# Optimization experiments

Hardware: AMD Instinct MI355X
Metric: run time of the kernel (lower is better)

The kernel has to match this reference:

```python
import jax, jax.numpy as jnp
import numpy as np

A_CONST = 0.4
C_CONST = 500.0
N_BINS = 10


def entropy(w):
    # Faithful to the torch helper: n=10 half-open bins [min+i*s, min+(i+1)*s);
    # the maximum element falls outside the last bin, as in the original.
    x = w.reshape(-1)
    lo = x.min()
    hi = x.max()
    scale = (hi - lo) / N_BINS
    i = jnp.arange(N_BINS, dtype=x.dtype)
    lower = lo + i * scale            # [n]
    upper = lo + (i + 1.0) * scale    # [n]
    in_bin = (x[None, :] >= lower[:, None]) & (x[None, :] < upper[:, None])  # [n, len]
    p = jnp.sum(in_bin, axis=1).astype(jnp.float32) / x.shape[0]
    return jnp.sum(jnp.where(p > 0, -p * jnp.log(p), 0.0))


def blend_weight(base_w, graft_w, pnet_w):
    # param_direction = |base - graft| passed through bias-free Linear(in, in)
    d = jnp.abs(base_w - graft_w) @ pnet_w.T          # [out, in]
    w_local = jax.nn.sigmoid(d)
    w_global = A_CONST / jnp.pi * jnp.arctan(C_CONST * (entropy(base_w) - entropy(graft_w))) + 0.5
    w_base = w_global * (1.0 - jnp.exp(-w_global * w_local))
    w_graft = (1.0 - w_global) * (1.0 - jnp.exp(-(1.0 - w_global) * (1.0 - w_local)))
    ws = jax.nn.softmax(jnp.stack([w_base, w_graft], axis=-1), axis=-1)  # [out, in, 2]
    return base_w * ws[..., 0] + graft_w * ws[..., 1]


def setup_inputs() -> dict:
    key = jax.random.key(0)
    ks = jax.random.split(key, 9)
    B, D_IN, D_H, D_OUT = 65536, 1024, 512, 1
    return {
        "x": jax.random.normal(ks[0], (B, D_IN), dtype=jnp.float32),
        "w0": jax.random.normal(ks[1], (D_H, D_IN), dtype=jnp.float32) * 0.05,
        "b0": jax.random.normal(ks[2], (D_H,), dtype=jnp.float32) * 0.05,
        "w1": jax.random.normal(ks[3], (D_OUT, D_H), dtype=jnp.float32) * 0.05,
        "b1": jax.random.normal(ks[4], (D_OUT,), dtype=jnp.float32) * 0.05,
        "p0": jax.random.normal(ks[5], (D_IN, D_IN), dtype=jnp.float32) * 0.05,
        "p1": jax.random.normal(ks[6], (D_H, D_H), dtype=jnp.float32) * 0.05,
        "g0": jax.random.normal(ks[7], (D_H, D_IN), dtype=jnp.float32) * 0.05,
        "g1": jax.random.normal(ks[8], (D_OUT, D_H), dtype=jnp.float32) * 0.05,
    }


def reference(x, w0, b0, w1, b1, p0, p1, g0, g1):
    W0 = blend_weight(w0, g0, p0)
    x = jax.nn.relu(x @ W0.T + b0)   # layer 0 + ReLU
    W1 = blend_weight(w1, g1, p1)
    x = x @ W1.T + b1                # layer 1, no activation
    return x
```

## Files before the change

kernel.cpp:

```cpp
#include <hip/hip_runtime.h>
#include <hip/hip_bf16.h>
#include <math.h>


typedef __attribute__((ext_vector_type(8))) short short8;
typedef __attribute__((ext_vector_type(4))) short short4v;
typedef __attribute__((ext_vector_type(4))) float floatx4;
typedef unsigned short ushort_t;

#define WS_ENT 0
#define WS_MM 4
#define WS_CNT 16
#define WS_W0B_WORD 64
#define WS_W1B_WORD (64 + 262144)

__device__ __forceinline__ unsigned f2ord(float f) {
    unsigned u = __float_as_uint(f);
    return (u & 0x80000000u) ? ~u : (u | 0x80000000u);
}
__device__ __forceinline__ float ord2f(unsigned k) {
    unsigned u = (k & 0x80000000u) ? (k ^ 0x80000000u) : ~k;
    return __uint_as_float(u);
}
__device__ __forceinline__ short f2bf(float f) {
    union { __hip_bfloat16 h; short s; } u;
    u.h = __float2bfloat16(f);
    return u.s;
}
__device__ __forceinline__ float blend_factor(float d, float wg) {
    float wl = 1.0f / (1.0f + expf(-d));
    float wb = wg * (1.0f - expf(-wg * wl));
    float wgr = (1.0f - wg) * (1.0f - expf(-(1.0f - wg) * (1.0f - wl)));
    return 1.0f / (1.0f + expf(-(wb - wgr)));
}
__device__ __forceinline__ float wglobal_from_ent(float eb, float eg) {
    return 0.12732395447351627f * atanf(500.0f * (eb - eg)) + 0.5f;
}
__device__ __forceinline__ void async16(const void* g, void* s) {
    __builtin_amdgcn_global_load_lds(
        (const __attribute__((address_space(1))) unsigned int*)g,
        (__attribute__((address_space(3))) unsigned int*)s, 16, 0, 0);
}

__global__ void init_ws(unsigned* ws_u) {
    int t = threadIdx.x;
    if (t < 4) {
        ws_u[WS_MM + 2 * t] = 0xFFFFFFFFu;
        ws_u[WS_MM + 2 * t + 1] = 0u;
    }
    if (t >= WS_CNT && t < WS_CNT + 40) ws_u[t] = 0u;
}

__device__ __forceinline__ void array_map(int bx, const float* w0, const float* g0,
                                          const float* w1, const float* g1,
                                          int& a, const float*& arr, int& per, int& start) {
    if (bx < 64) { a = 0; arr = w0; per = 524288 / 64; start = bx * per; }
    else if (bx < 128) { a = 1; arr = g0; per = 524288 / 64; start = (bx - 64) * per; }
    else if (bx == 128) { a = 2; arr = w1; per = 512; start = 0; }
    else { a = 3; arr = g1; per = 512; start = 0; }
}

__global__ __launch_bounds__(256) void minmax_kernel(const float* __restrict__ w0,
                                                     const float* __restrict__ g0,
                                                     const float* __restrict__ w1,
                                                     const float* __restrict__ g1,
                                                     unsigned* ws_u) {
    int a, per, start;
    const float* arr;
    array_map(blockIdx.x, w0, g0, w1, g1, a, arr, per, start);
    float mn = INFINITY, mx = -INFINITY;
    for (int i = threadIdx.x; i < per; i += 256) {
        float v = arr[start + i];
        mn = fminf(mn, v);
        mx = fmaxf(mx, v);
    }
#pragma unroll
    for (int off = 32; off > 0; off >>= 1) {
        mn = fminf(mn, __shfl_xor(mn, off));
        mx = fmaxf(mx, __shfl_xor(mx, off));
    }
    __shared__ float smn[4], smx[4];
    int wave = threadIdx.x >> 6, lane = threadIdx.x & 63;
    if (lane == 0) { smn[wave] = mn; smx[wave] = mx; }
    __syncthreads();
    if (threadIdx.x == 0) {
        mn = fminf(fminf(smn[0], smn[1]), fminf(smn[2], smn[3]));
        mx = fmaxf(fmaxf(smx[0], smx[1]), fmaxf(smx[2], smx[3]));
        atomicMin(&ws_u[WS_MM + 2 * a], f2ord(mn));
        atomicMax(&ws_u[WS_MM + 2 * a + 1], f2ord(mx));
    }
}

__global__ __launch_bounds__(256) void hist_kernel(const float* __restrict__ w0,
                                                   const float* __restrict__ g0,
                                                   const float* __restrict__ w1,
                                                   const float* __restrict__ g1,
                                                   unsigned* ws_u) {
    int a, per, start;
    const float* arr;
    array_map(blockIdx.x, w0, g0, w1, g1, a, arr, per, start);
    float lo = ord2f(ws_u[WS_MM + 2 * a]);
    float hi = ord2f(ws_u[WS_MM + 2 * a + 1]);
    float scale = __fdiv_rn(__fsub_rn(hi, lo), 10.0f);
    float lw[11];
#pragma unroll
    for (int j = 0; j < 11; j++)
        lw[j] = __fadd_rn(lo, __fmul_rn((float)j, scale));
    unsigned c[10];
#pragma unroll
    for (int b = 0; b < 10; b++) c[b] = 0u;
    for (int i = threadIdx.x; i < per; i += 256) {
        float v = arr[start + i];
#pragma unroll
        for (int b = 0; b < 10; b++)
            c[b] += (v >= lw[b] && v < lw[b + 1]) ? 1u : 0u;
    }
#pragma unroll
    for (int b = 0; b < 10; b++) {
#pragma unroll
        for (int off = 32; off > 0; off >>= 1) c[b] += __shfl_xor(c[b], off);
    }
    int lane = threadIdx.x & 63;
    if (lane == 0) {
#pragma unroll
        for (int b = 0; b < 10; b++)
            if (c[b] > 0u) atomicAdd(&ws_u[WS_CNT + a * 10 + b], c[b]);
    }
}

__global__ void finalize_ent_kernel(unsigned* ws_u) {
    int a = threadIdx.x;
    if (a < 4) {
        float n = (a < 2) ? 524288.0f : 512.0f;
        float ent = 0.0f;
        for (int i = 0; i < 10; i++) {
            float p = __fdiv_rn((float)ws_u[WS_CNT + a * 10 + i], n);
            if (p > 0.0f) ent = __fsub_rn(ent, __fmul_rn(p, logf(p)));
        }
        ((float*)ws_u)[WS_ENT + a] = ent;
    }
}

__global__ __launch_bounds__(256) void blend0_kernel(const float* __restrict__ w0,
                                                     const float* __restrict__ g0,
                                                     const float* __restrict__ p0,
                                                     const float* __restrict__ ws_f,
                                                     ushort_t* __restrict__ W0bb) {
    __shared__ ushort_t As[32 * 40];
    __shared__ ushort_t Ps[64 * 40];
    int tid = threadIdx.x;
    int w = tid >> 6, l = tid & 63;
    int bo = blockIdx.y * 32;
    int bi = blockIdx.x * 64;
    int wo = w & 1, wi = w >> 1;
    int m_in = l & 15, kq = l >> 4;

    floatx4 acc[2];
    const floatx4 zero = {0.0f, 0.0f, 0.0f, 0.0f};
    acc[0] = zero; acc[1] = zero;

    int ar = tid >> 3, ac = (tid & 7) * 4;
    int pr = tid >> 2, pc = (tid & 3) * 8;
    const float* wbase = w0 + (size_t)(bo + ar) * 1024 + ac;
    const float* gbase = g0 + (size_t)(bo + ar) * 1024 + ac;
    const float* pbase = p0 + (size_t)(bi + pr) * 1024 + pc;
    ushort_t* awr = &As[ar * 40 + ac];
    ushort_t* pwr = &Ps[pr * 40 + pc];

#pragma unroll 1
    for (int k0 = 0; k0 < 1024; k0 += 32) {
        float4 vw = *(const float4*)(wbase + k0);
        float4 vg = *(const float4*)(gbase + k0);
        float4 q0 = *(const float4*)(pbase + k0);
        float4 q1 = *(const float4*)(pbase + k0 + 4);
        short4v a4;
        a4[0] = f2bf(fabsf(vw.x - vg.x));
        a4[1] = f2bf(fabsf(vw.y - vg.y));
        a4[2] = f2bf(fabsf(vw.z - vg.z));
        a4[3] = f2bf(fabsf(vw.w - vg.w));
        short8 p8;
        p8[0] = f2bf(q0.x); p8[1] = f2bf(q0.y); p8[2] = f2bf(q0.z); p8[3] = f2bf(q0.w);
        p8[4] = f2bf(q1.x); p8[5] = f2bf(q1.y); p8[6] = f2bf(q1.z); p8[7] = f2bf(q1.w);
        *(short4v*)awr = a4;
        *(short8*)pwr = p8;
        __syncthreads();
        short8 af = *(const short8*)&As[(wo * 16 + m_in) * 40 + kq * 8];
        short8 pf0 = *(const short8*)&Ps[(wi * 32 + m_in) * 40 + kq * 8];
        short8 pf1 = *(const short8*)&Ps[(wi * 32 + 16 + m_in) * 40 + kq * 8];
        acc[0] = __builtin_amdgcn_mfma_f32_16x16x32_bf16(af, pf0, acc[0], 0, 0, 0);
        acc[1] = __builtin_amdgcn_mfma_f32_16x16x32_bf16(af, pf1, acc[1], 0, 0, 0);
        __syncthreads();
    }
    float wg = wglobal_from_ent(ws_f[WS_ENT + 0], ws_f[WS_ENT + 1]);
#pragma unroll
    for (int tn = 0; tn < 2; tn++) {
#pragma unroll
        for (int reg = 0; reg < 4; reg++) {
            int o = bo + wo * 16 + kq * 4 + reg;
            int i = bi + wi * 32 + tn * 16 + m_in;
            float s0 = blend_factor(acc[tn][reg], wg);
            float v = w0[o * 1024 + i] * s0 + g0[o * 1024 + i] * (1.0f - s0);
            W0bb[o * 1024 + i] = (ushort_t)f2bf(v);
        }
    }
}

__global__ __launch_bounds__(256) void blend1_kernel(const float* __restrict__ w1,
                                                     const float* __restrict__ g1,
                                                     const float* __restrict__ p1,
                                                     const float* __restrict__ ws_f,
                                                     float* __restrict__ W1b) {
    __shared__ float diff[512];
    int tid = threadIdx.x;
    for (int i = tid; i < 512; i += 256) diff[i] = fabsf(w1[i] - g1[i]);
    __syncthreads();
    int wave = tid >> 6, lane = tid & 63;
    int i = blockIdx.x * 4 + wave;
    float acc = 0.0f;
#pragma unroll
    for (int j = 0; j < 8; j++) {
        int k = lane + 64 * j;
        acc += diff[k] * p1[i * 512 + k];
    }
#pragma unroll
    for (int off = 32; off > 0; off >>= 1) acc += __shfl_xor(acc, off);
    if (lane == 0) {
        float wg = wglobal_from_ent(ws_f[WS_ENT + 2], ws_f[WS_ENT + 3]);
        float s0 = blend_factor(acc, wg);
        W1b[i] = w1[i] * s0 + g1[i] * (1.0f - s0);
    }
}

__global__ __launch_bounds__(256, 2) void main_mfma(const float* __restrict__ x,
                                                    const float* __restrict__ b0,
                                                    const ushort_t* __restrict__ W0bb,
                                                    const float* __restrict__ W1b,
                                                    const float* __restrict__ b1,
                                                    float* __restrict__ out) {
    __shared__ ushort_t As[64 * 40];
    __shared__ ushort_t Bs[512 * 32];
    __shared__ float red[4][64];
    int tid = threadIdx.x;
    int w = tid >> 6, l = tid & 63;
    int row0 = blockIdx.x * 64;
    int m_in = l & 15, kq = l >> 4;

    floatx4 acc[4][8];
    const floatx4 zero = {0.0f, 0.0f, 0.0f, 0.0f};
#pragma unroll
    for (int tm = 0; tm < 4; tm++)
#pragma unroll
        for (int tn = 0; tn < 8; tn++) acc[tm][tn] = zero;

    int arow = tid >> 2, acol = (tid & 3) * 8;
    const float* xbase = x + (size_t)(row0 + arow) * 1024 + acol;
    ushort_t* awr = &As[arow * 40 + acol];
    const ushort_t* bsrc = W0bb + (size_t)(w * 16 + (l >> 2)) * 1024 + (l & 3) * 8;
    ushort_t* bdst = &Bs[w * 512];

    float4 pv0 = *(const float4*)(xbase);
    float4 pv1 = *(const float4*)(xbase + 4);

#pragma unroll 1
    for (int k0 = 0; k0 < 1024; k0 += 32) {
#pragma unroll
        for (int r = 0; r < 8; r++)
            async16(bsrc + r * 65536 + k0, bdst + r * 2048);
        short8 s0;
        s0[0] = f2bf(pv0.x); s0[1] = f2bf(pv0.y); s0[2] = f2bf(pv0.z); s0[3] = f2bf(pv0.w);
        s0[4] = f2bf(pv1.x); s0[5] = f2bf(pv1.y); s0[6] = f2bf(pv1.z); s0[7] = f2bf(pv1.w);
        *(short8*)awr = s0;
        int kn = (k0 + 32 < 1024) ? k0 + 32 : 0;
        __syncthreads();
        pv0 = *(const float4*)(xbase + kn);
        pv1 = *(const float4*)(xbase + kn + 4);
        short8 af[4];
#pragma unroll
        for (int tm = 0; tm < 4; tm++)
            af[tm] = *(const short8*)&As[(tm * 16 + m_in) * 40 + kq * 8];
#pragma unroll
        for (int tn = 0; tn < 8; tn++) {
            short8 bfr = *(const short8*)&Bs[(w * 128 + tn * 16 + m_in) * 32 + kq * 8];
#pragma unroll
            for (int tm = 0; tm < 4; tm++)
                acc[tm][tn] = __builtin_amdgcn_mfma_f32_16x16x32_bf16(
                    af[tm], bfr, acc[tm][tn], 0, 0, 0);
        }
        __syncthreads();
    }

    float b0v[8], w1v[8];
#pragma unroll
    for (int tn = 0; tn < 8; tn++) {
        int h = w * 128 + tn * 16 + m_in;
        b0v[tn] = b0[h];
        w1v[tn] = W1b[h];
    }
#pragma unroll
    for (int tm = 0; tm < 4; tm++) {
#pragma unroll
        for (int reg = 0; reg < 4; reg++) {
            float s = 0.0f;
#pragma unroll
            for (int tn = 0; tn < 8; tn++) {
                float y = acc[tm][tn][reg] + b0v[tn];
                y = fmaxf(y, 0.0f);
                s += y * w1v[tn];
            }
            s += __shfl_xor(s, 1);
            s += __shfl_xor(s, 2);
            s += __shfl_xor(s, 4);
            s += __shfl_xor(s, 8);
            if (m_in == 0) red[w][tm * 16 + kq * 4 + reg] = s;
        }
    }
    __syncthreads();
    if (tid < 64)
        out[row0 + tid] = red[0][tid] + red[1][tid] + red[2][tid] + red[3][tid] + b1[0];
}

extern "C" void kernel_launch(void* const* d_in, const int* in_sizes, int n_in,
                              void* d_out, int out_size, void* d_ws, size_t ws_size,
                              hipStream_t stream) {
    const float* x = (const float*)d_in[0];
    const float* w0 = (const float*)d_in[1];
    const float* b0 = (const float*)d_in[2];
    const float* w1 = (const float*)d_in[3];
    const float* b1 = (const float*)d_in[4];
    const float* p0 = (const float*)d_in[5];
    const float* p1 = (const float*)d_in[6];
    const float* g0 = (const float*)d_in[7];
    const float* g1 = (const float*)d_in[8];
    float* out = (float*)d_out;
    unsigned* ws_u = (unsigned*)d_ws;
    float* ws_f = (float*)d_ws;
    ushort_t* W0bb = (ushort_t*)(ws_u + WS_W0B_WORD);
    float* W1b = ws_f + WS_W1B_WORD;

    init_ws<<<1, 64, 0, stream>>>(ws_u);
    minmax_kernel<<<130, 256, 0, stream>>>(w0, g0, w1, g1, ws_u);
    hist_kernel<<<130, 256, 0, stream>>>(w0, g0, w1, g1, ws_u);
    finalize_ent_kernel<<<1, 64, 0, stream>>>(ws_u);
    blend0_kernel<<<dim3(16, 16), 256, 0, stream>>>(w0, g0, p0, ws_f, W0bb);
    blend1_kernel<<<128, 256, 0, stream>>>(w1, g1, p1, ws_f, W1b);
    main_mfma<<<1024, 256, 0, stream>>>(x, b0, W0bb, W1b, b1, out);
}
```

Measured before the change: 525.7 us.

## Fuse weight-prep kernels cooperatively, tile-transpose W0, double-buffer main GEMM

Merges the init, min/max, histogram, entropy and both blend kernels into one cooperative kernel with grid syncs, falling back to separate launches if the cooperative launch fails. The blended W0 is now written in a k-tile-major bf16 layout so each main-GEMM k-step loads one contiguous block. The main MFMA loop now double-buffers the A and B LDS tiles, prefetching the next tile while computing the current one, which removes one barrier per iteration. The aim is to cut launch overhead and hide load latency, at the cost of doubled LDS use, which may reduce occupancy under the two-blocks-per-CU launch bound.

```diff
diff --git a/kernel.cpp b/kernel.cpp
--- a/kernel.cpp
+++ b/kernel.cpp
@@ -1,5 +1,6 @@
 #include <hip/hip_runtime.h>
 #include <hip/hip_bf16.h>
+#include <hip/hip_cooperative_groups.h>
 #include <math.h>
 
 
@@ -42,116 +43,185 @@
         (__attribute__((address_space(3))) unsigned int*)s, 16, 0, 0);
 }
 
-__global__ void init_ws(unsigned* ws_u) {
-    int t = threadIdx.x;
-    if (t < 4) {
-        ws_u[WS_MM + 2 * t] = 0xFFFFFFFFu;
-        ws_u[WS_MM + 2 * t + 1] = 0u;
-    }
-    if (t >= WS_CNT && t < WS_CNT + 40) ws_u[t] = 0u;
-}
-
-__device__ __forceinline__ void array_map(int bx, const float* w0, const float* g0,
-                                          const float* w1, const float* g1,
-                                          int& a, const float*& arr, int& per, int& start) {
-    if (bx < 64) { a = 0; arr = w0; per = 524288 / 64; start = bx * per; }
-    else if (bx < 128) { a = 1; arr = g0; per = 524288 / 64; start = (bx - 64) * per; }
-    else if (bx == 128) { a = 2; arr = w1; per = 512; start = 0; }
-    else { a = 3; arr = g1; per = 512; start = 0; }
-}
-
-__global__ __launch_bounds__(256) void minmax_kernel(const float* __restrict__ w0,
-                                                     const float* __restrict__ g0,
-                                                     const float* __restrict__ w1,
-                                                     const float* __restrict__ g1,
-                                                     unsigned* ws_u) {
-    int a, per, start;
-    const float* arr;
-    array_map(blockIdx.x, w0, g0, w1, g1, a, arr, per, start);
+__device__ __forceinline__ void phase_init(int tid, unsigned* ws_u) {
+    if (tid < 4) {
+        ws_u[WS_MM + 2 * tid] = 0xFFFFFFFFu;
+        ws_u[WS_MM + 2 * tid + 1] = 0u;
+    }
+    if (tid >= WS_CNT && tid < WS_CNT + 40) ws_u[tid] = 0u;
+}
+
+__device__ __forceinline__ void phase_minmax(int bx, int tid,
+                                             const float* w0, const float* g0,
+                                             const float* w1, const float* g1,
+                                             unsigned* ws_u) {
+    __shared__ float smn[4], smx[4];
+    int wave = tid >> 6, lane = tid & 63;
+    int a = bx >> 7;
+    const float* arr = (a ? g0 : w0) + (size_t)(bx & 127) * 4096;
     float mn = INFINITY, mx = -INFINITY;
-    for (int i = threadIdx.x; i < per; i += 256) {
-        float v = arr[start + i];
-        mn = fminf(mn, v);
-        mx = fmaxf(mx, v);
+    const float4* p4 = (const float4*)arr;
+#pragma unroll
+    for (int j = 0; j < 4; j++) {
+        float4 v = p4[tid + j * 256];
+        mn = fminf(mn, fminf(fminf(v.x, v.y), fminf(v.z, v.w)));
+        mx = fmaxf(mx, fmaxf(fmaxf(v.x, v.y), fmaxf(v.z, v.w)));
     }
 #pragma unroll
     for (int off = 32; off > 0; off >>= 1) {
         mn = fminf(mn, __shfl_xor(mn, off));
         mx = fmaxf(mx, __shfl_xor(mx, off));
     }
-    __shared__ float smn[4], smx[4];
-    int wave = threadIdx.x >> 6, lane = threadIdx.x & 63;
     if (lane == 0) { smn[wave] = mn; smx[wave] = mx; }
     __syncthreads();
-    if (threadIdx.x == 0) {
+    if (tid == 0) {
         mn = fminf(fminf(smn[0], smn[1]), fminf(smn[2], smn[3]));
         mx = fmaxf(fmaxf(smx[0], smx[1]), fmaxf(smx[2], smx[3]));
         atomicMin(&ws_u[WS_MM + 2 * a], f2ord(mn));
         atomicMax(&ws_u[WS_MM + 2 * a + 1], f2ord(mx));
     }
-}
-
-__global__ __launch_bounds__(256) void hist_kernel(const float* __restrict__ w0,
-                                                   const float* __restrict__ g0,
-                                                   const float* __restrict__ w1,
-                                                   const float* __restrict__ g1,
-                                                   unsigned* ws_u) {
-    int a, per, start;
-    const float* arr;
-    array_map(blockIdx.x, w0, g0, w1, g1, a, arr, per, start);
-    float lo = ord2f(ws_u[WS_MM + 2 * a]);
-    float hi = ord2f(ws_u[WS_MM + 2 * a + 1]);
-    float scale = __fdiv_rn(__fsub_rn(hi, lo), 10.0f);
-    float lw[11];
-#pragma unroll
-    for (int j = 0; j < 11; j++)
-        lw[j] = __fadd_rn(lo, __fmul_rn((float)j, scale));
-    unsigned c[10];
-#pragma unroll
-    for (int b = 0; b < 10; b++) c[b] = 0u;
-    for (int i = threadIdx.x; i < per; i += 256) {
-        float v = arr[start + i];
-#pragma unroll
-        for (int b = 0; b < 10; b++)
-            c[b] += (v >= lw[b] && v < lw[b + 1]) ? 1u : 0u;
-    }
-#pragma unroll
-    for (int b = 0; b < 10; b++) {
-#pragma unroll
-        for (int off = 32; off > 0; off >>= 1) c[b] += __shfl_xor(c[b], off);
-    }
-    int lane = threadIdx.x & 63;
-    if (lane == 0) {
-#pragma unroll
-        for (int b = 0; b < 10; b++)
-            if (c[b] > 0u) atomicAdd(&ws_u[WS_CNT + a * 10 + b], c[b]);
-    }
-}
-
-__global__ void finalize_ent_kernel(unsigned* ws_u) {
-    int a = threadIdx.x;
-    if (a < 4) {
-        float n = (a < 2) ? 524288.0f : 512.0f;
+    if (bx < 2 && tid < 64) {
+        const float* arr2 = bx ? g1 : w1;
+        int a2 = 2 + bx;
+        float mn2 = INFINITY, mx2 = -INFINITY;
+#pragma unroll
+        for (int j = 0; j < 8; j++) {
+            float v = arr2[tid + 64 * j];
+            mn2 = fminf(mn2, v);
+            mx2 = fmaxf(mx2, v);
+        }
+#pragma unroll
+        for (int off = 32; off > 0; off >>= 1) {
+            mn2 = fminf(mn2, __shfl_xor(mn2, off));
+            mx2 = fmaxf(mx2, __shfl_xor(mx2, off));
+        }
+        if (tid == 0) {
+            atomicMin(&ws_u[WS_MM + 2 * a2], f2ord(mn2));
+            atomicMax(&ws_u[WS_MM + 2 * a2 + 1], f2ord(mx2));
+        }
+    }
+}
+
+__device__ __forceinline__ void phase_hist(int bx, int tid,
+                                           const float* w0, const float* g0,
+                                           const float* w1, const float* g1,
+                                           unsigned* ws_u) {
+    int lane = tid & 63;
+    {
+        int a = bx >> 7;
+        const float* arr = (a ? g0 : w0) + (size_t)(bx & 127) * 4096;
+        float lo = ord2f(ws_u[WS_MM + 2 * a]);
+        float hi = ord2f(ws_u[WS_MM + 2 * a + 1]);
+        float scale = __fdiv_rn(__fsub_rn(hi, lo), 10.0f);
+        float lw[11];
+#pragma unroll
+        for (int j = 0; j < 11; j++)
+            lw[j] = __fadd_rn(lo, __fmul_rn((float)j, scale));
+        unsigned c[10];
+#pragma unroll
+        for (int b = 0; b < 10; b++) c[b] = 0u;
+        const float4* p4 = (const float4*)arr;
+#pragma unroll
+        for (int j = 0; j < 4; j++) {
+            float4 v4 = p4[tid + j * 256];
+            float vv[4] = {v4.x, v4.y, v4.z, v4.w};
+#pragma unroll
+            for (int e = 0; e < 4; e++) {
+                float v = vv[e];
+#pragma unroll
+                for (int b = 0; b < 10; b++)
+                    c[b] += (v >= lw[b] && v < lw[b + 1]) ? 1u : 0u;
+            }
+        }
+#pragma unroll
+        for (int b = 0; b < 10; b++) {
+#pragma unroll
+            for (int off = 32; off > 0; off >>= 1) c[b] += __shfl_xor(c[b], off);
+        }
+        if (lane == 0) {
+#pragma unroll
+            for (int b = 0; b < 10; b++)
+                if (c[b] > 0u) atomicAdd(&ws_u[WS_CNT + a * 10 + b], c[b]);
+        }
+    }
+    if (bx < 2 && tid < 64) {
+        int a2 = 2 + bx;
+        const float* arr2 = bx ? g1 : w1;
+        float lo = ord2f(ws_u[WS_MM + 2 * a2]);
+        float hi = ord2f(ws_u[WS_MM + 2 * a2 + 1]);
+        float scale = __fdiv_rn(__fsub_rn(hi, lo), 10.0f);
+        float lw[11];
+#pragma unroll
+        for (int j = 0; j < 11; j++)
+            lw[j] = __fadd_rn(lo, __fmul_rn((float)j, scale));
+        unsigned c[10];
+#pragma unroll
+        for (int b = 0; b < 10; b++) c[b] = 0u;
+#pragma unroll
+        for (int j = 0; j < 8; j++) {
+            float v = arr2[tid + 64 * j];
+#pragma unroll
+            for (int b = 0; b < 10; b++)
+                c[b] += (v >= lw[b] && v < lw[b + 1]) ? 1u : 0u;
+        }
+#pragma unroll
+        for (int b = 0; b < 10; b++) {
+#pragma unroll
+            for (int off = 32; off > 0; off >>= 1) c[b] += __shfl_xor(c[b], off);
+        }
+        if (tid == 0) {
+#pragma unroll
+            for (int b = 0; b < 10; b++)
+                if (c[b] > 0u) atomicAdd(&ws_u[WS_CNT + a2 * 10 + b], c[b]);
+        }
+    }
+}
+
+__device__ __forceinline__ void phase_ent(int tid, unsigned* ws_u) {
+    if (tid < 4) {
+        float n = (tid < 2) ? 524288.0f : 512.0f;
         float ent = 0.0f;
         for (int i = 0; i < 10; i++) {
-            float p = __fdiv_rn((float)ws_u[WS_CNT + a * 10 + i], n);
+            float p = __fdiv_rn((float)ws_u[WS_CNT + tid * 10 + i], n);
             if (p > 0.0f) ent = __fsub_rn(ent, __fmul_rn(p, logf(p)));
         }
-        ((float*)ws_u)[WS_ENT + a] = ent;
-    }
-}
-
-__global__ __launch_bounds__(256) void blend0_kernel(const float* __restrict__ w0,
-                                                     const float* __restrict__ g0,
-                                                     const float* __restrict__ p0,
-                                                     const float* __restrict__ ws_f,
-                                                     ushort_t* __restrict__ W0bb) {
+        ((float*)ws_u)[WS_ENT + tid] = ent;
+    }
+}
+
+__device__ __forceinline__ void phase_blend1(int bx, int tid,
+                                             const float* w1, const float* g1,
+                                             const float* p1, const float* ws_f,
+                                             float* W1b) {
+    __shared__ float diff[512];
+    for (int i = tid; i < 512; i += 256) diff[i] = fabsf(w1[i] - g1[i]);
+    __syncthreads();
+    int wave = tid >> 6, lane = tid & 63;
+    int i = bx * 4 + wave;
+    float acc = 0.0f;
+#pragma unroll
+    for (int j = 0; j < 8; j++) {
+        int k = lane + 64 * j;
+        acc += diff[k] * p1[i * 512 + k];
+    }
+#pragma unroll
+    for (int off = 32; off > 0; off >>= 1) acc += __shfl_xor(acc, off);
+    if (lane == 0) {
+        float wg = wglobal_from_ent(ws_f[WS_ENT + 2], ws_f[WS_ENT + 3]);
+        float s0 = blend_factor(acc, wg);
+        W1b[i] = w1[i] * s0 + g1[i] * (1.0f - s0);
+    }
+}
+
+__device__ __forceinline__ void phase_blend0(int bx, int tid,
+                                             const float* w0, const float* g0,
+                                             const float* p0, const float* ws_f,
+                                             ushort_t* W0t) {
     __shared__ ushort_t As[32 * 40];
     __shared__ ushort_t Ps[64 * 40];
-    int tid = threadIdx.x;
     int w = tid >> 6, l = tid & 63;
-    int bo = blockIdx.y * 32;
-    int bi = blockIdx.x * 64;
+    int bo = (bx >> 4) * 32;
+    int bi = (bx & 15) * 64;
     int wo = w & 1, wi = w >> 1;
     int m_in = l & 15, kq = l >> 4;
 
@@ -200,45 +270,75 @@
             int i = bi + wi * 32 + tn * 16 + m_in;
             float s0 = blend_factor(acc[tn][reg], wg);
             float v = w0[o * 1024 + i] * s0 + g0[o * 1024 + i] * (1.0f - s0);
-            W0bb[o * 1024 + i] = (ushort_t)f2bf(v);
-        }
-    }
-}
-
-__global__ __launch_bounds__(256) void blend1_kernel(const float* __restrict__ w1,
-                                                     const float* __restrict__ g1,
-                                                     const float* __restrict__ p1,
-                                                     const float* __restrict__ ws_f,
-                                                     float* __restrict__ W1b) {
-    __shared__ float diff[512];
-    int tid = threadIdx.x;
-    for (int i = tid; i < 512; i += 256) diff[i] = fabsf(w1[i] - g1[i]);
-    __syncthreads();
-    int wave = tid >> 6, lane = tid & 63;
-    int i = blockIdx.x * 4 + wave;
-    float acc = 0.0f;
-#pragma unroll
-    for (int j = 0; j < 8; j++) {
-        int k = lane + 64 * j;
-        acc += diff[k] * p1[i * 512 + k];
-    }
-#pragma unroll
-    for (int off = 32; off > 0; off >>= 1) acc += __shfl_xor(acc, off);
-    if (lane == 0) {
-        float wg = wglobal_from_ent(ws_f[WS_ENT + 2], ws_f[WS_ENT + 3]);
-        float s0 = blend_factor(acc, wg);
-        W1b[i] = w1[i] * s0 + g1[i] * (1.0f - s0);
-    }
+            W0t[(size_t)(i >> 5) * 16384 + o * 32 + (i & 31)] = (ushort_t)f2bf(v);
+        }
+    }
+}
+
+__global__ __launch_bounds__(256) void prep_coop(const float* w0, const float* g0,
+                                                 const float* w1, const float* g1,
+                                                 const float* p0, const float* p1,
+                                                 unsigned* ws_u, ushort_t* W0t,
+                                                 float* W1b) {
+    cooperative_groups::grid_group grid = cooperative_groups::this_grid();
+    int bx = blockIdx.x, tid = threadIdx.x;
+    if (bx == 0) phase_init(tid, ws_u);
+    __threadfence();
+    grid.sync();
+    phase_minmax(bx, tid, w0, g0, w1, g1, ws_u);
+    __threadfence();
+    grid.sync();
+    phase_hist(bx, tid, w0, g0, w1, g1, ws_u);
+    __threadfence();
+    grid.sync();
+    if (bx == 0) phase_ent(tid, ws_u);
+    __threadfence();
+    grid.sync();
+    if (bx < 128) phase_blend1(bx, tid, w1, g1, p1, (const float*)ws_u, W1b);
+    phase_blend0(bx, tid, w0, g0, p0, (const float*)ws_u, W0t);
+}
+
+__global__ __launch_bounds__(256) void k_init(unsigned* ws_u) {
+    phase_init(threadIdx.x, ws_u);
+}
+__global__ __launch_bounds__(256) void k_minmax(const float* __restrict__ w0,
+                                                const float* __restrict__ g0,
+                                                const float* __restrict__ w1,
+                                                const float* __restrict__ g1,
+                                                unsigned* ws_u) {
+    phase_minmax(blockIdx.x, threadIdx.x, w0, g0, w1, g1, ws_u);
+}
+__global__ __launch_bounds__(256) void k_hist(const float* __restrict__ w0,
+                                              const float* __restrict__ g0,
+                                              const float* __restrict__ w1,
+                                              const float* __restrict__ g1,
+                                              unsigned* ws_u) {
+    phase_hist(blockIdx.x, threadIdx.x, w0, g0, w1, g1, ws_u);
+}
+__global__ void k_ent(unsigned* ws_u) { phase_ent(threadIdx.x, ws_u); }
+__global__ __launch_bounds__(256) void k_blend1(const float* __restrict__ w1,
+                                                const float* __restrict__ g1,
+                                                const float* __restrict__ p1,
+                                                const float* __restrict__ ws_f,
+                                                float* __restrict__ W1b) {
+    phase_blend1(blockIdx.x, threadIdx.x, w1, g1, p1, ws_f, W1b);
+}
+__global__ __launch_bounds__(256) void k_blend0(const float* __restrict__ w0,
+                                                const float* __restrict__ g0,
+                                                const float* __restrict__ p0,
+                                                const float* __restrict__ ws_f,
+                                                ushort_t* __restrict__ W0t) {
+    phase_blend0(blockIdx.x, threadIdx.x, w0, g0, p0, ws_f, W0t);
 }
 
 __global__ __launch_bounds__(256, 2) void main_mfma(const float* __restrict__ x,
                                                     const float* __restrict__ b0,
-                                                    const ushort_t* __restrict__ W0bb,
+                                                    const ushort_t* __restrict__ W0t,
                                                     const float* __restrict__ W1b,
                                                     const float* __restrict__ b1,
                                                     float* __restrict__ out) {
-    __shared__ ushort_t As[64 * 40];
-    __shared__ ushort_t Bs[512 * 32];
+    __shared__ ushort_t As[2][64 * 40];
+    __shared__ ushort_t Bs[2][512 * 32];
     __shared__ float red[4][64];
     int tid = threadIdx.x;
     int w = tid >> 6, l = tid & 63;
@@ -254,37 +354,52 @@
 
     int arow = tid >> 2, acol = (tid & 3) * 8;
     const float* xbase = x + (size_t)(row0 + arow) * 1024 + acol;
-    ushort_t* awr = &As[arow * 40 + acol];
-    const ushort_t* bsrc = W0bb + (size_t)(w * 16 + (l >> 2)) * 1024 + (l & 3) * 8;
-    ushort_t* bdst = &Bs[w * 512];
+    int awr_off = arow * 40 + acol;
+    const ushort_t* bsrc = W0t + (size_t)tid * 8;
 
     float4 pv0 = *(const float4*)(xbase);
     float4 pv1 = *(const float4*)(xbase + 4);
-
-#pragma unroll 1
-    for (int k0 = 0; k0 < 1024; k0 += 32) {
-#pragma unroll
-        for (int r = 0; r < 8; r++)
-            async16(bsrc + r * 65536 + k0, bdst + r * 2048);
+#pragma unroll
+    for (int r = 0; r < 8; r++)
+        async16(bsrc + r * 2048, &Bs[0][r * 2048 + w * 512]);
+    {
         short8 s0;
         s0[0] = f2bf(pv0.x); s0[1] = f2bf(pv0.y); s0[2] = f2bf(pv0.z); s0[3] = f2bf(pv0.w);
         s0[4] = f2bf(pv1.x); s0[5] = f2bf(pv1.y); s0[6] = f2bf(pv1.z); s0[7] = f2bf(pv1.w);
-        *(short8*)awr = s0;
-        int kn = (k0 + 32 < 1024) ? k0 + 32 : 0;
-        __syncthreads();
-        pv0 = *(const float4*)(xbase + kn);
-        pv1 = *(const float4*)(xbase + kn + 4);
+        *(short8*)&As[0][awr_off] = s0;
+    }
+    __syncthreads();
+
+#pragma unroll 1
+    for (int t = 0; t < 32; ++t) {
+        int cur = t & 1, nxt = cur ^ 1;
+        float4 nv0, nv1;
+        if (t < 31) {
+            const float* xn = xbase + (t + 1) * 32;
+            nv0 = *(const float4*)xn;
+            nv1 = *(const float4*)(xn + 4);
+            const ushort_t* bt = bsrc + (t + 1) * 16384;
+#pragma unroll
+            for (int r = 0; r < 8; r++)
+                async16(bt + r * 2048, &Bs[nxt][r * 2048 + w * 512]);
+        }
         short8 af[4];
 #pragma unroll
         for (int tm = 0; tm < 4; tm++)
-            af[tm] = *(const short8*)&As[(tm * 16 + m_in) * 40 + kq * 8];
+            af[tm] = *(const short8*)&As[cur][(tm * 16 + m_in) * 40 + kq * 8];
 #pragma unroll
         for (int tn = 0; tn < 8; tn++) {
-            short8 bfr = *(const short8*)&Bs[(w * 128 + tn * 16 + m_in) * 32 + kq * 8];
+            short8 bfr = *(const short8*)&Bs[cur][(w * 128 + tn * 16 + m_in) * 32 + kq * 8];
 #pragma unroll
             for (int tm = 0; tm < 4; tm++)
                 acc[tm][tn] = __builtin_amdgcn_mfma_f32_16x16x32_bf16(
                     af[tm], bfr, acc[tm][tn], 0, 0, 0);
+        }
+        if (t < 31) {
+            short8 s0;
+            s0[0] = f2bf(nv0.x); s0[1] = f2bf(nv0.y); s0[2] = f2bf(nv0.z); s0[3] = f2bf(nv0.w);
+            s0[4] = f2bf(nv1.x); s0[5] = f2bf(nv1.y); s0[6] = f2bf(nv1.z); s0[7] = f2bf(nv1.w);
+            *(short8*)&As[nxt][awr_off] = s0;
         }
         __syncthreads();
     }
@@ -334,14 +449,20 @@
     float* out = (float*)d_out;
     unsigned* ws_u = (unsigned*)d_ws;
     float* ws_f = (float*)d_ws;
-    ushort_t* W0bb = (ushort_t*)(ws_u + WS_W0B_WORD);
+    ushort_t* W0t = (ushort_t*)(ws_u + WS_W0B_WORD);
     float* W1b = ws_f + WS_W1B_WORD;
 
-    init_ws<<<1, 64, 0, stream>>>(ws_u);
-    minmax_kernel<<<130, 256, 0, stream>>>(w0, g0, w1, g1, ws_u);
-    hist_kernel<<<130, 256, 0, stream>>>(w0, g0, w1, g1, ws_u);
-    finalize_ent_kernel<<<1, 64, 0, stream>>>(ws_u);
-    blend0_kernel<<<dim3(16, 16), 256, 0, stream>>>(w0, g0, p0, ws_f, W0bb);
-    blend1_kernel<<<128, 256, 0, stream>>>(w1, g1, p1, ws_f, W1b);
-    main_mfma<<<1024, 256, 0, stream>>>(x, b0, W0bb, W1b, b1, out);
-}
+    void* args[] = {(void*)&w0, (void*)&g0, (void*)&w1, (void*)&g1,
+                    (void*)&p0, (void*)&p1, (void*)&ws_u, (void*)&W0t, (void*)&W1b};
+    hipError_t ce = hipLaunchCooperativeKernel((const void*)prep_coop, dim3(256),
+                                               dim3(256), args, 0, stream);
+    if (ce != hipSuccess) {
+        k_init<<<1, 256, 0, stream>>>(ws_u);
+        k_minmax<<<256, 256, 0, stream>>>(w0, g0, w1, g1, ws_u);
+        k_hist<<<256, 256, 0, stream>>>(w0, g0, w1, g1, ws_u);
+        k_ent<<<1, 64, 0, stream>>>(ws_u);
+        k_blend1<<<128, 256, 0, stream>>>(w1, g1, p1, ws_f, W1b);
+        k_blend0<<<256, 256, 0, stream>>>(w0, g0, p0, ws_f, W0t);
+    }
+    main_mfma<<<1024, 256, 0, stream>>>(x, b0, W0t, W1b, b1, out);
+}
```

New measurement: 724.0 us. +37.7%, slower.
